# Optimization experiments

Hardware: AMD Instinct MI355X
Metric: run time of the kernel (lower is better)

## Reference

```python
import jax, jax.numpy as jnp
import numpy as np

CODEBOOK_SIZE = 1024
CODEBOOK_DIM = 256
MUSIC_WEIGHT = 0.1
EPS_COS = 1e-8


def setup_inputs() -> dict:
    key = jax.random.key(0)
    k1, k2, k3, k4 = jax.random.split(key, 4)
    B, D, T = 16, CODEBOOK_DIM, 2048
    x = jax.random.normal(k1, (B, D, T), dtype=jnp.float32)
    music_context = jax.random.normal(k2, (B, 3, T), dtype=jnp.float32)
    # codebook initialized uniform(-1/K, 1/K) as in the torch module
    codebook = jax.random.uniform(k3, (CODEBOOK_SIZE, D), dtype=jnp.float32,
                                  minval=-1.0 / CODEBOOK_SIZE, maxval=1.0 / CODEBOOK_SIZE)
    w_proj = jax.random.normal(k4, (3, D), dtype=jnp.float32) * (1.0 / np.sqrt(D))
    b_proj = jnp.zeros((3,), dtype=jnp.float32)
    return {"x": x, "music_context": music_context, "codebook": codebook,
            "w_proj": w_proj, "b_proj": b_proj}


def reference(x, music_context, codebook, w_proj, b_proj):
    B, D, T = x.shape
    K = codebook.shape[0]
    sg = jax.lax.stop_gradient

    # ---- VQ: nearest-codebook lookup (eval mode, no EMA update) ----
    x_flat = jnp.transpose(x, (0, 2, 1)).reshape(-1, D)             # [B*T, D]
    # squared euclidean distances; argmin equals argmin of cdist
    d2 = (jnp.sum(x_flat * x_flat, axis=1, keepdims=True)
          - 2.0 * (x_flat @ codebook.T)
          + jnp.sum(codebook * codebook, axis=1))                    # [B*T, K]
    codes = jnp.argmin(d2, axis=1)                                   # [B*T]
    q_flat = codebook[codes]                                         # [B*T, D] gather
    quantized = jnp.transpose(q_flat.reshape(B, T, D), (0, 2, 1))    # [B, D, T]

    commitment_loss = jnp.mean((sg(quantized) - x) ** 2)
    codebook_loss = jnp.mean((quantized - sg(x)) ** 2)
    quantized_st = x + sg(quantized - x)                             # straight-through

    # ---- perplexity of code usage ----
    counts = jnp.zeros((K,), dtype=jnp.float32).at[codes].add(1.0)
    avg_probs = counts / codes.shape[0]
    perplexity = jnp.exp(-jnp.sum(avg_probs * jnp.log(avg_probs + 1e-10)))

    # ---- music-aware consistency loss (vectorized over time) ----
    music_proj = x_flat @ w_proj.T + b_proj                          # [B*T, 3]
    music_proj = jnp.transpose(music_proj.reshape(B, T, 3), (0, 2, 1))  # [B, 3, T]
    num = jnp.sum(music_proj * music_context, axis=1)                # [B, T]
    np_norm = jnp.maximum(jnp.linalg.norm(music_proj, axis=1), EPS_COS)
    nc_norm = jnp.maximum(jnp.linalg.norm(music_context, axis=1), EPS_COS)
    music_sim = num / (np_norm * nc_norm)                            # [B, T]

    codes_bt = codes.reshape(B, T)
    sim_diff = jnp.abs(music_sim[:, 1:] - music_sim[:, :-1])         # [B, T-1]
    code_diff = (codes_bt[:, 1:] != codes_bt[:, :-1]).astype(jnp.float32)
    # sum over t of mean over batch, divided by (T-1) == global mean
    music_loss = jnp.mean(sim_diff * code_diff)

    commitment_total = commitment_loss + MUSIC_WEIGHT * music_loss
    return (quantized_st, codes_bt, commitment_total, codebook_loss, perplexity, music_loss)
```

## Files before the change

kernel.cpp:

```cpp
#include <hip/hip_runtime.h>
#include <hip/hip_bf16.h>
#include <math.h>

#define B_    16
#define D_    256
#define T_    2048
#define K_    1024
#define BT_   (B_ * T_)
#define BDT_  (B_ * D_ * T_)
#define MUSIC_W 0.1f
#define EPS_COS 1e-8f
#define MARGIN_TAU 2e-4f

typedef _Float16 half8v __attribute__((ext_vector_type(8)));
typedef float f32x4 __attribute__((ext_vector_type(4)));

__device__ __forceinline__ float pw128_sq(const float* a, int stride) {
    float r[8];
    #pragma unroll
    for (int j = 0; j < 8; ++j) { float v = a[j * stride]; r[j] = __fmul_rn(v, v); }
    for (int i = 8; i < 128; i += 8) {
        #pragma unroll
        for (int j = 0; j < 8; ++j) {
            float v = a[(i + j) * stride];
            r[j] = __fadd_rn(r[j], __fmul_rn(v, v));
        }
    }
    return __fadd_rn(__fadd_rn(__fadd_rn(r[0], r[1]), __fadd_rn(r[2], r[3])),
                     __fadd_rn(__fadd_rn(r[4], r[5]), __fadd_rn(r[6], r[7])));
}
__device__ __forceinline__ float pw256_sq(const float* a, int stride) {
    return __fadd_rn(pw128_sq(a, stride), pw128_sq(a + 128 * stride, stride));
}

__device__ __forceinline__ float np_score(const float* __restrict__ xr,
                                          const float* __restrict__ cp,
                                          float xxv, float c2k) {
    double a0 = 0.0, a1 = 0.0, a2 = 0.0, a3 = 0.0;
    for (int d = 0; d < 256; d += 4) {
        float4 cv = *(const float4*)(cp + d);
        a0 = fma((double)xr[d + 0], (double)cv.x, a0);
        a1 = fma((double)xr[d + 1], (double)cv.y, a1);
        a2 = fma((double)xr[d + 2], (double)cv.z, a2);
        a3 = fma((double)xr[d + 3], (double)cv.w, a3);
    }
    float M = (float)((a0 + a1) + (a2 + a3));
    return __fadd_rn(__fsub_rn(xxv, __fmul_rn(2.0f, M)), c2k);
}

__device__ __forceinline__ unsigned key_fwd(float s) {
    unsigned u = __float_as_uint(s);
    return u ^ ((unsigned)((int)u >> 31) | 0x80000000u);
}
__device__ __forceinline__ float key_inv(unsigned key) {
    unsigned u = (key & 0x80000000u) ? (key ^ 0x80000000u) : ~key;
    return __uint_as_float(u);
}

#define PREPK 16

__global__ __launch_bounds__(256) void prep_kernel(const float* __restrict__ cb,
                                                   const float* __restrict__ wp,
                                                   _Float16* __restrict__ cph,
                                                   _Float16* __restrict__ wh,
                                                   float* __restrict__ c2,
                                                   float* __restrict__ counts,
                                                   double* __restrict__ sums,
                                                   int* __restrict__ ticket) {
    __shared__ float cbl[PREPK * 256];
    int k0 = blockIdx.x * PREPK;
    int tid = threadIdx.x;

    #pragma unroll
    for (int kk = 0; kk < PREPK; ++kk)
        cbl[kk * 256 + tid] = cb[(size_t)(k0 + kk) * D_ + tid];
    __syncthreads();

    if (tid < PREPK) {
        c2[k0 + tid] = pw256_sq(&cbl[tid * 256], 1);
        counts[k0 + tid] = 0.0f;
    }

    #pragma unroll
    for (int pp = 0; pp < 2; ++pp) {
        int p = tid + pp * 256;
        int o = p >> 4, kk = p & 15;
        half8v h;
        #pragma unroll
        for (int j = 0; j < 8; ++j) h[j] = (_Float16)cbl[kk * 256 + o * 8 + j];
        *(half8v*)&cph[((size_t)o * K_ + (k0 + kk)) * 8] = h;
    }

    if (blockIdx.x == 0) {
        int d = tid;
        #pragma unroll
        for (int kw = 0; kw < 16; ++kw) {
            _Float16 hv = (kw < 3) ? (_Float16)wp[kw * D_ + d] : (_Float16)0.0f;
            wh[((d >> 3) * 16 + kw) * 8 + (d & 7)] = hv;
        }
        if (tid < 2) sums[tid] = 0.0;
        if (tid == 2) *ticket = 0;
    }
}

#define HSTR 264

__global__ __launch_bounds__(256, 2) void argmin_kernel(const float* __restrict__ x,
                                                        const float* __restrict__ mc,
                                                        const float* __restrict__ bp,
                                                        const _Float16* __restrict__ cph,
                                                        const _Float16* __restrict__ wh,
                                                        const float* __restrict__ cb,
                                                        const float* __restrict__ c2,
                                                        int* __restrict__ codes,
                                                        float* __restrict__ codes_f,
                                                        float* __restrict__ sim,
                                                        float* __restrict__ counts,
                                                        float* __restrict__ out0,
                                                        double* __restrict__ sums) {
    __shared__ __align__(16) _Float16 xh[64 * HSTR];
    __shared__ __align__(16) float xrow[256];
    __shared__ unsigned wb1[4][64], wb2[4][64];
    __shared__ float rbest[64];
    __shared__ int   rcode[64];
    __shared__ int   fb_list[64];
    __shared__ int   fb_n;
    __shared__ float fbv_s[4];
    __shared__ int   fbk_s[4];
    __shared__ float bs[3];
    __shared__ float qpart[4];

    int blk = blockIdx.x;
    int row0 = blk * 64;
    int b = row0 >> 11;
    int t0 = row0 & 2047;
    const float* xb = x + (size_t)b * (D_ * T_);

    int tid = threadIdx.x;
    if (tid == 0) fb_n = 0;
    if (tid < 3) bs[tid] = bp[tid];

    int wave = tid >> 6;
    int lane = tid & 63;
    int lmod = lane & 15;
    int lgrp = lane >> 4;

    half8v bfrA[8], bfrB[8];
    {
        int n = wave * 256 + lmod;
        #pragma unroll
        for (int kb = 0; kb < 8; ++kb)
            bfrA[kb] = *(const half8v*)(cph + ((size_t)((kb << 2) + lgrp) * K_ + n) * 8);
    }
    float c2cur = c2[wave * 256 + lmod];

    int li = tid & 63;
    int dhi = tid >> 6;
    #pragma unroll
    for (int q = 0; q < 8; ++q) {
        half8v hv;
        #pragma unroll
        for (int j = 0; j < 8; ++j) {
            float v = xb[(size_t)(dhi * 64 + q * 8 + j) * T_ + t0 + li];
            hv[j] = (_Float16)v;
        }
        *(half8v*)&xh[li * HSTR + dhi * 64 + q * 8] = hv;
    }
    __syncthreads();

    half8v afrag[2][8];
    #pragma unroll
    for (int mt = 0; mt < 2; ++mt)
        #pragma unroll
        for (int kb = 0; kb < 8; ++kb)
            afrag[mt][kb] = *(const half8v*)&xh[(mt * 16 + lmod) * HSTR + lgrp * 8 + kb * 32];

    unsigned b1[16], b2[16];
    #pragma unroll
    for (int r = 0; r < 16; ++r) { b1[r] = 0xFFFFFFFFu; b2[r] = 0xFFFFFFFFu; }

    #pragma unroll 1
    for (int nt = 0; nt < 16; ++nt) {
        int n = wave * 256 + nt * 16 + lmod;
        float c2nxt = 0.0f;
        if (nt < 15) {
            int n2 = n + 16;
            #pragma unroll
            for (int kb = 0; kb < 8; ++kb)
                bfrB[kb] = *(const half8v*)(cph + ((size_t)((kb << 2) + lgrp) * K_ + n2) * 8);
            c2nxt = c2[n2];
        }
        float c2n = c2cur;
        #pragma unroll
        for (int mt = 0; mt < 2; ++mt) {
            f32x4 acc = {0.f, 0.f, 0.f, 0.f};
            #pragma unroll
            for (int kb = 0; kb < 8; ++kb)
                acc = __builtin_amdgcn_mfma_f32_16x16x32_f16(afrag[mt][kb], bfrA[kb], acc, 0, 0, 0);
            #pragma unroll
            for (int i = 0; i < 4; ++i) {
                float s = fmaf(-2.0f, acc[i], c2n);
                unsigned u = (key_fwd(s) & 0xFFFFFC00u) | (unsigned)n;
                int r = mt * 4 + i;
                unsigned mx = b1[r] > u ? b1[r] : u;
                b1[r] = b1[r] < u ? b1[r] : u;
                b2[r] = b2[r] < mx ? b2[r] : mx;
            }
        }
        #pragma unroll
        for (int mt = 2; mt < 4; ++mt) {
            f32x4 acc = {0.f, 0.f, 0.f, 0.f};
            #pragma unroll
            for (int kb = 0; kb < 8; ++kb) {
                half8v av = *(const half8v*)&xh[(mt * 16 + lmod) * HSTR + lgrp * 8 + kb * 32];
                acc = __builtin_amdgcn_mfma_f32_16x16x32_f16(av, bfrA[kb], acc, 0, 0, 0);
            }
            #pragma unroll
            for (int i = 0; i < 4; ++i) {
                float s = fmaf(-2.0f, acc[i], c2n);
                unsigned u = (key_fwd(s) & 0xFFFFFC00u) | (unsigned)n;
                int r = mt * 4 + i;
                unsigned mx = b1[r] > u ? b1[r] : u;
                b1[r] = b1[r] < u ? b1[r] : u;
                b2[r] = b2[r] < mx ? b2[r] : mx;
            }
        }
        #pragma unroll
        for (int kb = 0; kb < 8; ++kb) bfrA[kb] = bfrB[kb];
        c2cur = c2nxt;
    }

    #pragma unroll
    for (int r = 0; r < 16; ++r) {
        unsigned v1 = b1[r], v2 = b2[r];
        #pragma unroll
        for (int off = 1; off < 16; off <<= 1) {
            unsigned o1 = (unsigned)__shfl_xor((int)v1, off, 64);
            unsigned o2 = (unsigned)__shfl_xor((int)v2, off, 64);
            unsigned mx = v1 > o1 ? v1 : o1;
            v1 = v1 < o1 ? v1 : o1;
            unsigned m2 = v2 < o2 ? v2 : o2;
            v2 = m2 < mx ? m2 : mx;
        }
        if (lmod == 0) {
            int row = (r >> 2) * 16 + lgrp * 4 + (r & 3);
            wb1[wave][row] = v1; wb2[wave][row] = v2;
        }
    }
    __syncthreads();

    if (tid < 64) {
        unsigned B1 = wb1[0][tid], B2 = wb2[0][tid];
        #pragma unroll
        for (int w = 1; w < 4; ++w) {
            unsigned o1 = wb1[w][tid], o2 = wb2[w][tid];
            unsigned mx = B1 > o1 ? B1 : o1;
            B1 = B1 < o1 ? B1 : o1;
            unsigned m2 = B2 < o2 ? B2 : o2;
            B2 = m2 < mx ? m2 : mx;
        }
        float f1 = key_inv(B1 & 0xFFFFFC00u);
        float f2 = key_inv(B2 & 0xFFFFFC00u);
        rbest[tid] = f1;
        int row = row0 + tid;
        if (f2 - f1 >= MARGIN_TAU) {
            int bk = (int)(B1 & 1023u);
            rcode[tid] = bk;
            codes[row] = bk;
            codes_f[row] = (float)bk;
            atomicAdd(&counts[bk], 1.0f);
        } else {
            int slot = atomicAdd(&fb_n, 1);
            fb_list[slot] = tid;
        }
    }
    __syncthreads();

    int nf = fb_n;
    for (int fi = 0; fi < nf; ++fi) {
        int lr = fb_list[fi];
        float rb = rbest[lr];
        xrow[tid] = xb[(size_t)tid * T_ + t0 + lr];
        __syncthreads();

        int ri = (((lr >> 2) & 3) == lgrp) ? ((lr >> 4) * 4 + (lr & 3)) : -1;
        unsigned k1 = 0xFFFFFFFFu, k2 = 0xFFFFFFFFu;
        #pragma unroll
        for (int r = 0; r < 16; ++r) {
            if (r == ri) { k1 = b1[r]; k2 = b2[r]; }
        }
        float f1s = key_inv(k1 & 0xFFFFFC00u);
        float f2s = key_inv(k2 & 0xFFFFFC00u);
        int f1k = (int)(k1 & 1023u), f2k = (int)(k2 & 1023u);

        float xxv = pw256_sq(xrow, 1);

        float bv = 3.4e38f; int bk = -1;
        if (ri >= 0 && f1s <= rb + MARGIN_TAU) {
            bv = np_score(xrow, cb + (size_t)f1k * D_, xxv, c2[f1k]);
            bk = f1k;
        }
        if (ri >= 0 && f2s <= rb + MARGIN_TAU) {
            float sB = np_score(xrow, cb + (size_t)f2k * D_, xxv, c2[f2k]);
            if (sB < bv || (sB == bv && (unsigned)f2k < (unsigned)bk)) { bv = sB; bk = f2k; }
        }
        #pragma unroll
        for (int off = 1; off < 64; off <<= 1) {
            float ov = __shfl_xor(bv, off, 64);
            int ok = __shfl_xor(bk, off, 64);
            if (ov < bv || (ov == bv && (unsigned)ok < (unsigned)bk)) { bv = ov; bk = ok; }
        }
        if (lane == 0) { fbv_s[wave] = bv; fbk_s[wave] = bk; }
        __syncthreads();
        if (tid == 0) {
            float Bv = fbv_s[0]; int Bk = fbk_s[0];
            #pragma unroll
            for (int w = 1; w < 4; ++w) {
                if (fbv_s[w] < Bv || (fbv_s[w] == Bv && (unsigned)fbk_s[w] < (unsigned)Bk)) {
                    Bv = fbv_s[w]; Bk = fbk_s[w];
                }
            }
            rcode[lr] = Bk;
            codes[row0 + lr] = Bk;
            codes_f[row0 + lr] = (float)Bk;
            atomicAdd(&counts[Bk], 1.0f);
        }
        __syncthreads();
    }
    __syncthreads();

    {
        int mt = wave;
        f32x4 am = {0.f, 0.f, 0.f, 0.f};
        #pragma unroll
        for (int kb = 0; kb < 8; ++kb) {
            half8v av = *(const half8v*)&xh[(mt * 16 + lmod) * HSTR + lgrp * 8 + kb * 32];
            half8v wf = *(const half8v*)(wh + (((size_t)((kb << 2) + lgrp)) * 16 + lmod) * 8);
            am = __builtin_amdgcn_mfma_f32_16x16x32_f16(av, wf, am, 0, 0, 0);
        }
        float bias = (lmod < 3) ? bs[lmod] : 0.0f;
        #pragma unroll
        for (int i = 0; i < 4; ++i) {
            float m = am[i] + bias;
            float m1 = __shfl_down(m, 1, 64);
            float m2 = __shfl_down(m, 2, 64);
            if (lmod == 0) {
                int row = mt * 16 + lgrp * 4 + i;
                const float* mcp = mc + (size_t)b * (3 * T_) + (t0 + row);
                float c0 = mcp[0], c1v = mcp[T_], c2v = mcp[2 * T_];
                float num = m * c0 + m1 * c1v + m2 * c2v;
                float npn = fmaxf(sqrtf(m * m + m1 * m1 + m2 * m2), EPS_COS);
                float ncn = fmaxf(sqrtf(c0 * c0 + c1v * c1v + c2v * c2v), EPS_COS);
                sim[row0 + row] = num / (npn * ncn);
            }
        }
    }

    {
        const float* cbr = cb + (size_t)rcode[li] * D_;
        float* outb = out0 + (size_t)b * (D_ * T_) + t0 + li;
        float part = 0.0f;
        #pragma unroll 2
        for (int ch = 0; ch < 8; ++ch) {
            int d0 = dhi * 64 + ch * 8;
            half8v xv8 = *(const half8v*)&xh[li * HSTR + d0];
            float4 qa = *(const float4*)(cbr + d0);
            float4 qb = *(const float4*)(cbr + d0 + 4);
            float qs[8] = {qa.x, qa.y, qa.z, qa.w, qb.x, qb.y, qb.z, qb.w};
            #pragma unroll
            for (int j = 0; j < 8; ++j) {
                outb[(size_t)(d0 + j) * T_] = qs[j];
                float df = qs[j] - (float)xv8[j];
                part = fmaf(df, df, part);
            }
        }
        #pragma unroll
        for (int off = 32; off; off >>= 1) part += __shfl_down(part, off, 64);
        if (lane == 0) qpart[wave] = part;
        __syncthreads();
        if (tid == 0) {
            double s = (double)qpart[0] + qpart[1] + qpart[2] + qpart[3];
            atomicAdd(&sums[0], s);
        }
    }
}

__global__ __launch_bounds__(256) void mloss_final(const float* __restrict__ sim,
                                                   const int* __restrict__ codes,
                                                   const float* __restrict__ counts,
                                                   double* __restrict__ sums,
                                                   float* __restrict__ outS,
                                                   int* __restrict__ ticket) {
    __shared__ float part[4];
    __shared__ int is_last;
    int tid = threadIdx.x;
    int lane = tid & 63, wv = tid >> 6;

    int idx = blockIdx.x * 256 + tid;
    float val = 0.0f;
    if (idx < B_ * (T_ - 1)) {
        int b = idx / (T_ - 1);
        int t = idx - b * (T_ - 1);
        int base = b * T_ + t;
        if (codes[base + 1] != codes[base])
            val = fabsf(sim[base + 1] - sim[base]);
    }
    #pragma unroll
    for (int off = 32; off; off >>= 1) val += __shfl_down(val, off, 64);
    if (lane == 0) part[wv] = val;
    __syncthreads();
    if (tid == 0) {
        double s = (double)part[0] + part[1] + part[2] + part[3];
        atomicAdd(&sums[1], s);
        __threadfence();
        is_last = (atomicAdd(ticket, 1) == (int)gridDim.x - 1) ? 1 : 0;
    }
    __syncthreads();
    if (!is_last) return;

    float e = 0.0f;
    for (int k = tid; k < K_; k += 256) {
        float p = counts[k] * (1.0f / (float)BT_);
        e += p * logf(p + 1e-10f);
    }
    #pragma unroll
    for (int off = 32; off; off >>= 1) e += __shfl_down(e, off, 64);
    if (lane == 0) part[wv] = e;
    __syncthreads();
    if (tid == 0) {
        float etot = part[0] + part[1] + part[2] + part[3];
        float perp = expf(-etot);
        double s0 = atomicAdd(&sums[0], 0.0);
        double s1 = atomicAdd(&sums[1], 0.0);
        float commitment = (float)(s0 / (double)BDT_);
        float ml = (float)(s1 / (double)(B_ * (T_ - 1)));
        outS[0] = commitment + MUSIC_W * ml;
        outS[1] = commitment;
        outS[2] = perp;
        outS[3] = ml;
    }
}

extern "C" void kernel_launch(void* const* d_in, const int* in_sizes, int n_in,
                              void* d_out, int out_size, void* d_ws, size_t ws_size,
                              hipStream_t stream) {
    const float* x   = (const float*)d_in[0];
    const float* mc  = (const float*)d_in[1];
    const float* cb  = (const float*)d_in[2];
    const float* wp  = (const float*)d_in[3];
    const float* bp  = (const float*)d_in[4];

    float* wsf = (float*)d_ws;
    double* sums     = (double*)wsf;
    float* c2        = wsf + 4;
    float* sim       = c2 + K_;
    float* counts    = sim + BT_;
    int*   codes     = (int*)(counts + K_);
    _Float16* cph    = (_Float16*)(codes + BT_);
    _Float16* wh     = cph + (size_t)D_ * K_;
    int*   ticket    = (int*)(wh + 2048);

    float* out0    = (float*)d_out;
    float* codes_f = out0 + BDT_;
    float* outS    = codes_f + BT_;

    prep_kernel<<<K_ / PREPK, 256, 0, stream>>>(cb, wp, cph, wh, c2, counts, sums, ticket);
    argmin_kernel<<<BT_ / 64, 256, 0, stream>>>(x, mc, bp, cph, wh, cb, c2,
                                                codes, codes_f, sim, counts, out0, sums);
    mloss_final<<<(B_ * (T_ - 1) + 255) / 256, 256, 0, stream>>>(sim, codes, counts,
                                                                 sums, outS, ticket);
}
```

Before: 91.46 us.

## Halve rows per block to 32 and drop codebook register double-buffering

Each argmin block now handles 32 rows instead of 64, which doubles the grid and keeps all A fragments in registers rather than re-reading half of them from LDS. The codebook B-fragment software prefetch (double buffer) is removed, and fragments are loaded at the top of each iteration. This lowers register and LDS pressure to improve occupancy and parallelism. In exchange, each codebook tile is reused across fewer rows, so codebook traffic from L2 doubles and load latency is no longer hidden by explicit prefetch.

```diff
diff --git a/kernel.cpp b/kernel.cpp
--- a/kernel.cpp
+++ b/kernel.cpp
@@ -118,12 +118,12 @@
                                                         float* __restrict__ counts,
                                                         float* __restrict__ out0,
                                                         double* __restrict__ sums) {
-    __shared__ __align__(16) _Float16 xh[64 * HSTR];
+    __shared__ __align__(16) _Float16 xh[32 * HSTR];
     __shared__ __align__(16) float xrow[256];
-    __shared__ unsigned wb1[4][64], wb2[4][64];
-    __shared__ float rbest[64];
-    __shared__ int   rcode[64];
-    __shared__ int   fb_list[64];
+    __shared__ unsigned wb1[4][32], wb2[4][32];
+    __shared__ float rbest[32];
+    __shared__ int   rcode[32];
+    __shared__ int   fb_list[32];
     __shared__ int   fb_n;
     __shared__ float fbv_s[4];
     __shared__ int   fbk_s[4];
@@ -131,7 +131,7 @@
     __shared__ float qpart[4];
 
     int blk = blockIdx.x;
-    int row0 = blk * 64;
+    int row0 = blk * 32;
     int b = row0 >> 11;
     int t0 = row0 & 2047;
     const float* xb = x + (size_t)b * (D_ * T_);
@@ -145,26 +145,17 @@
     int lmod = lane & 15;
     int lgrp = lane >> 4;
 
-    half8v bfrA[8], bfrB[8];
-    {
-        int n = wave * 256 + lmod;
-        #pragma unroll
-        for (int kb = 0; kb < 8; ++kb)
-            bfrA[kb] = *(const half8v*)(cph + ((size_t)((kb << 2) + lgrp) * K_ + n) * 8);
-    }
-    float c2cur = c2[wave * 256 + lmod];
-
-    int li = tid & 63;
-    int dhi = tid >> 6;
-    #pragma unroll
-    for (int q = 0; q < 8; ++q) {
+    int li = tid & 31;
+    int dseg = tid >> 5;
+    #pragma unroll
+    for (int q = 0; q < 4; ++q) {
         half8v hv;
         #pragma unroll
         for (int j = 0; j < 8; ++j) {
-            float v = xb[(size_t)(dhi * 64 + q * 8 + j) * T_ + t0 + li];
+            float v = xb[(size_t)(dseg * 32 + q * 8 + j) * T_ + t0 + li];
             hv[j] = (_Float16)v;
         }
-        *(half8v*)&xh[li * HSTR + dhi * 64 + q * 8] = hv;
+        *(half8v*)&xh[li * HSTR + dseg * 32 + q * 8] = hv;
     }
     __syncthreads();
 
@@ -175,28 +166,24 @@
         for (int kb = 0; kb < 8; ++kb)
             afrag[mt][kb] = *(const half8v*)&xh[(mt * 16 + lmod) * HSTR + lgrp * 8 + kb * 32];
 
-    unsigned b1[16], b2[16];
-    #pragma unroll
-    for (int r = 0; r < 16; ++r) { b1[r] = 0xFFFFFFFFu; b2[r] = 0xFFFFFFFFu; }
+    unsigned b1[8], b2[8];
+    #pragma unroll
+    for (int r = 0; r < 8; ++r) { b1[r] = 0xFFFFFFFFu; b2[r] = 0xFFFFFFFFu; }
 
     #pragma unroll 1
     for (int nt = 0; nt < 16; ++nt) {
         int n = wave * 256 + nt * 16 + lmod;
-        float c2nxt = 0.0f;
-        if (nt < 15) {
-            int n2 = n + 16;
-            #pragma unroll
-            for (int kb = 0; kb < 8; ++kb)
-                bfrB[kb] = *(const half8v*)(cph + ((size_t)((kb << 2) + lgrp) * K_ + n2) * 8);
-            c2nxt = c2[n2];
-        }
-        float c2n = c2cur;
+        half8v bfr[8];
+        #pragma unroll
+        for (int kb = 0; kb < 8; ++kb)
+            bfr[kb] = *(const half8v*)(cph + ((size_t)((kb << 2) + lgrp) * K_ + n) * 8);
+        float c2n = c2[n];
         #pragma unroll
         for (int mt = 0; mt < 2; ++mt) {
             f32x4 acc = {0.f, 0.f, 0.f, 0.f};
             #pragma unroll
             for (int kb = 0; kb < 8; ++kb)
-                acc = __builtin_amdgcn_mfma_f32_16x16x32_f16(afrag[mt][kb], bfrA[kb], acc, 0, 0, 0);
+                acc = __builtin_amdgcn_mfma_f32_16x16x32_f16(afrag[mt][kb], bfr[kb], acc, 0, 0, 0);
             #pragma unroll
             for (int i = 0; i < 4; ++i) {
                 float s = fmaf(-2.0f, acc[i], c2n);
@@ -207,31 +194,10 @@
                 b2[r] = b2[r] < mx ? b2[r] : mx;
             }
         }
-        #pragma unroll
-        for (int mt = 2; mt < 4; ++mt) {
-            f32x4 acc = {0.f, 0.f, 0.f, 0.f};
-            #pragma unroll
-            for (int kb = 0; kb < 8; ++kb) {
-                half8v av = *(const half8v*)&xh[(mt * 16 + lmod) * HSTR + lgrp * 8 + kb * 32];
-                acc = __builtin_amdgcn_mfma_f32_16x16x32_f16(av, bfrA[kb], acc, 0, 0, 0);
-            }
-            #pragma unroll
-            for (int i = 0; i < 4; ++i) {
-                float s = fmaf(-2.0f, acc[i], c2n);
-                unsigned u = (key_fwd(s) & 0xFFFFFC00u) | (unsigned)n;
-                int r = mt * 4 + i;
-                unsigned mx = b1[r] > u ? b1[r] : u;
-                b1[r] = b1[r] < u ? b1[r] : u;
-                b2[r] = b2[r] < mx ? b2[r] : mx;
-            }
-        }
-        #pragma unroll
-        for (int kb = 0; kb < 8; ++kb) bfrA[kb] = bfrB[kb];
-        c2cur = c2nxt;
-    }
-
-    #pragma unroll
-    for (int r = 0; r < 16; ++r) {
+    }
+
+    #pragma unroll
+    for (int r = 0; r < 8; ++r) {
         unsigned v1 = b1[r], v2 = b2[r];
         #pragma unroll
         for (int off = 1; off < 16; off <<= 1) {
@@ -249,7 +215,7 @@
     }
     __syncthreads();
 
-    if (tid < 64) {
+    if (tid < 32) {
         unsigned B1 = wb1[0][tid], B2 = wb2[0][tid];
         #pragma unroll
         for (int w = 1; w < 4; ++w) {
@@ -286,7 +252,7 @@
         int ri = (((lr >> 2) & 3) == lgrp) ? ((lr >> 4) * 4 + (lr & 3)) : -1;
         unsigned k1 = 0xFFFFFFFFu, k2 = 0xFFFFFFFFu;
         #pragma unroll
-        for (int r = 0; r < 16; ++r) {
+        for (int r = 0; r < 8; ++r) {
             if (r == ri) { k1 = b1[r]; k2 = b2[r]; }
         }
         float f1s = key_inv(k1 & 0xFFFFFC00u);
@@ -329,14 +295,13 @@
     }
     __syncthreads();
 
-    {
+    if (wave < 2) {
         int mt = wave;
         f32x4 am = {0.f, 0.f, 0.f, 0.f};
         #pragma unroll
         for (int kb = 0; kb < 8; ++kb) {
-            half8v av = *(const half8v*)&xh[(mt * 16 + lmod) * HSTR + lgrp * 8 + kb * 32];
             half8v wf = *(const half8v*)(wh + (((size_t)((kb << 2) + lgrp)) * 16 + lmod) * 8);
-            am = __builtin_amdgcn_mfma_f32_16x16x32_f16(av, wf, am, 0, 0, 0);
+            am = __builtin_amdgcn_mfma_f32_16x16x32_f16(afrag[mt][kb], wf, am, 0, 0, 0);
         }
         float bias = (lmod < 3) ? bs[lmod] : 0.0f;
         #pragma unroll
@@ -360,9 +325,9 @@
         const float* cbr = cb + (size_t)rcode[li] * D_;
         float* outb = out0 + (size_t)b * (D_ * T_) + t0 + li;
         float part = 0.0f;
-        #pragma unroll 2
-        for (int ch = 0; ch < 8; ++ch) {
-            int d0 = dhi * 64 + ch * 8;
+        #pragma unroll
+        for (int ch = 0; ch < 4; ++ch) {
+            int d0 = dseg * 32 + ch * 8;
             half8v xv8 = *(const half8v*)&xh[li * HSTR + d0];
             float4 qa = *(const float4*)(cbr + d0);
             float4 qb = *(const float4*)(cbr + d0 + 4);
@@ -465,7 +430,7 @@
     float* outS    = codes_f + BT_;
 
     prep_kernel<<<K_ / PREPK, 256, 0, stream>>>(cb, wp, cph, wh, c2, counts, sums, ticket);
-    argmin_kernel<<<BT_ / 64, 256, 0, stream>>>(x, mc, bp, cph, wh, cb, c2,
+    argmin_kernel<<<BT_ / 32, 256, 0, stream>>>(x, mc, bp, cph, wh, cb, c2,
                                                 codes, codes_f, sim, counts, out0, sums);
     mloss_final<<<(B_ * (T_ - 1) + 255) / 256, 256, 0, stream>>>(sim, codes, counts,
                                                                  sums, outS, ticket);
```

After: 147.4 us. 61.2% more time.
